# Kernel tuning notes

Hardware: AMD Instinct MI355X
Metric: run time of the kernel (lower is better)

Reference implementation:

```python
import jax, jax.numpy as jnp
import numpy as np

N = 50000      # nodes
E = 800000     # edges (avg degree 16)
EL = 200000    # link-prediction pairs
IN = 128       # in_channels
HID = 128      # hidden_conv_2


def setup_inputs() -> dict:
    key = jax.random.key(0)
    ks = jax.random.split(key, 12)
    x = jax.random.normal(ks[0], (N, IN), dtype=jnp.float32)
    edge_index = jax.random.randint(ks[1], (2, E), 0, N, dtype=jnp.int64)
    edge_label_index = jax.random.randint(ks[2], (2, EL), 0, N, dtype=jnp.int64)
    H = jnp.zeros((N, HID), dtype=jnp.float32)
    s_in = 1.0 / np.sqrt(IN)
    s_h = 1.0 / np.sqrt(HID)
    # Stacked ChebConv (K=2) weights for gates [z, r, h]:
    # Wx*: convs on the input x (IN -> HID); Wh*: convs on the state H (HID -> HID)
    Wx0 = jax.random.uniform(ks[3], (3, IN, HID), jnp.float32, -s_in, s_in)
    Wx1 = jax.random.uniform(ks[4], (3, IN, HID), jnp.float32, -s_in, s_in)
    bx = jax.random.uniform(ks[5], (3, HID), jnp.float32, -s_in, s_in)
    Wh0 = jax.random.uniform(ks[6], (3, HID, HID), jnp.float32, -s_h, s_h)
    Wh1 = jax.random.uniform(ks[7], (3, HID, HID), jnp.float32, -s_h, s_h)
    bh = jax.random.uniform(ks[8], (3, HID), jnp.float32, -s_h, s_h)
    post_w = jax.random.uniform(ks[9], (HID, 2), jnp.float32, -s_h, s_h)
    post_b = jax.random.uniform(ks[10], (2,), jnp.float32, -s_h, s_h)
    return {"x": x, "edge_index": edge_index, "edge_label_index": edge_label_index,
            "H": H, "Wx0": Wx0, "Wx1": Wx1, "bx": bx,
            "Wh0": Wh0, "Wh1": Wh1, "bh": bh,
            "post_w": post_w, "post_b": post_b}


def _gconv_gru(x, H, edge_index, Wx0, Wx1, bx, Wh0, Wh1, bh):
    src, dst = edge_index[0], edge_index[1]
    # Symmetric-normalized ChebConv edge weights with lambda_max=2:
    # L_hat = L - I = -D^{-1/2} A D^{-1/2}
    deg = jax.ops.segment_sum(jnp.ones(src.shape[0], x.dtype), src, num_segments=N)
    dinv = jnp.where(deg > 0, jax.lax.rsqrt(jnp.maximum(deg, 1e-12)), 0.0)
    norm = -(dinv[src] * dinv[dst])  # [E]

    def prop(v):  # L_hat @ v via gather-scale-scatter
        return jax.ops.segment_sum(v[src] * norm[:, None], dst, num_segments=N)

    px = prop(x)   # shared Tx_1 for all three x-convs
    pH = prop(H)

    def cheb_x(g):
        return x @ Wx0[g] + px @ Wx1[g] + bx[g]

    def cheb_h(v, pv, g):
        return v @ Wh0[g] + pv @ Wh1[g] + bh[g]

    Z = jax.nn.sigmoid(cheb_x(0) + cheb_h(H, pH, 0))
    R = jax.nn.sigmoid(cheb_x(1) + cheb_h(H, pH, 1))
    HR = H * R
    Ht = jnp.tanh(cheb_x(2) + cheb_h(HR, prop(HR), 2))
    return Z * H + (1.0 - Z) * Ht


def reference(x, edge_index, edge_label_index, H,
              Wx0, Wx1, bx, Wh0, Wh1, bh, post_w, post_b):
    h = _gconv_gru(x, H, edge_index, Wx0, Wx1, bx, Wh0, Wh1, bh)
    hidden = h  # detached copy in the original
    hr = jax.nn.relu(h)
    h_src = hr[edge_label_index[0]]  # [EL, HID]
    h_dst = hr[edge_label_index[1]]
    had = h_src * h_dst
    scores = jnp.sum(had @ post_w + post_b, axis=-1)  # [EL]
    return scores, hidden
```

## Files before the change

kernel.cpp:

```cpp
#include <hip/hip_runtime.h>

#define N_NODES 50000
#define N_EDGES 800000
#define N_EL    200000
#define CH      128
#define NTILES  3125

typedef __attribute__((ext_vector_type(8))) short bf16x8;
typedef __attribute__((ext_vector_type(4))) float f32x4;

__device__ __forceinline__ unsigned short f2bf(float f){
  unsigned int u = __float_as_uint(f);
  unsigned int r = (u + 0x7fff + ((u >> 16) & 1)) >> 16;
  return (unsigned short)r;
}
__device__ __forceinline__ float bflo(unsigned int v){ return __uint_as_float(v << 16); }
__device__ __forceinline__ float bfhi(unsigned int v){ return __uint_as_float(v & 0xffff0000u); }
__device__ __forceinline__ float bf2f(unsigned short u){ return __uint_as_float(((unsigned int)u) << 16); }

__global__ void hist_kernel(const int* __restrict__ ei, int* deg, int* cnt){
  int i = blockIdx.x*blockDim.x + threadIdx.x;
  if (i < N_EDGES){
    atomicAdd(&deg[ei[i]], 1);
    atomicAdd(&cnt[ei[N_EDGES + i]], 1);
  }
}

__global__ void dinv_kernel(const int* __restrict__ deg, float* __restrict__ dinv){
  int i = blockIdx.x*blockDim.x + threadIdx.x;
  if (i < N_NODES){
    int d = deg[i];
    dinv[i] = d > 0 ? rsqrtf((float)d) : 0.0f;
  }
}

#define SCAN_NB 196

__global__ void scan_bsum(const int* __restrict__ cnt, int* __restrict__ bsum){
  __shared__ int sh[256];
  int i = blockIdx.x*256 + threadIdx.x;
  sh[threadIdx.x] = (i < N_NODES) ? cnt[i] : 0;
  __syncthreads();
  for (int off = 128; off >= 1; off >>= 1){
    if ((int)threadIdx.x < off) sh[threadIdx.x] += sh[threadIdx.x + off];
    __syncthreads();
  }
  if (threadIdx.x == 0) bsum[blockIdx.x] = sh[0];
}

__global__ void scan_boff(const int* __restrict__ bsum, int* __restrict__ boff){
  __shared__ int sh[256];
  int t = threadIdx.x;
  int v = (t < SCAN_NB) ? bsum[t] : 0;
  sh[t] = v;
  __syncthreads();
  for (int off = 1; off < 256; off <<= 1){
    int tv = (t >= off) ? sh[t - off] : 0;
    __syncthreads();
    sh[t] += tv;
    __syncthreads();
  }
  if (t < SCAN_NB) boff[t] = sh[t] - v;
}

__global__ void scan_final(const int* __restrict__ cnt, const int* __restrict__ boff,
                           int* __restrict__ rowoff, int* __restrict__ cursor){
  __shared__ int sh[256];
  int t = threadIdx.x;
  int i = blockIdx.x*256 + t;
  int v = (i < N_NODES) ? cnt[i] : 0;
  sh[t] = v;
  __syncthreads();
  for (int off = 1; off < 256; off <<= 1){
    int tv = (t >= off) ? sh[t - off] : 0;
    __syncthreads();
    sh[t] += tv;
    __syncthreads();
  }
  int o = boff[blockIdx.x] + sh[t] - v;
  if (i < N_NODES){ rowoff[i] = o; cursor[i] = o; }
  if (i == N_NODES - 1) rowoff[N_NODES] = N_EDGES;
}

__global__ void scatter_kernel(const int* __restrict__ ei, const float* __restrict__ dinv,
                               int* cursor, int* __restrict__ csr_src,
                               float* __restrict__ csr_norm){
  int i = blockIdx.x*blockDim.x + threadIdx.x;
  if (i < N_EDGES){
    int s = ei[i];
    int d = ei[N_EDGES + i];
    int pos = atomicAdd(&cursor[d], 1);
    csr_src[pos]  = s;
    csr_norm[pos] = -(dinv[s] * dinv[d]);
  }
}

__global__ void cvt_xH(const float* __restrict__ x, const float* __restrict__ H,
                       unsigned short* __restrict__ xH){
  const int Q = (N_NODES*CH)/4;
  int i = blockIdx.x*blockDim.x + threadIdx.x;
  if (i >= 2*Q) return;
  const float* src = (i < Q) ? x : H;
  int off = (i < Q) ? i : i - Q;
  float4 v = ((const float4*)src)[off];
  int node = off >> 5, cg = off & 31;
  uint2 o;
  o.x = (unsigned int)f2bf(v.x) | ((unsigned int)f2bf(v.y) << 16);
  o.y = (unsigned int)f2bf(v.z) | ((unsigned int)f2bf(v.w) << 16);
  *(uint2*)(xH + (size_t)node*256 + ((i < Q) ? 0 : 128) + cg*4) = o;
}

__global__ void cvt_w(const float* __restrict__ Wx0, const float* __restrict__ Wx1,
                      const float* __restrict__ Wh0, const float* __restrict__ Wh1,
                      unsigned short* __restrict__ wt){
  int i = blockIdx.x*blockDim.x + threadIdx.x;
  if (i >= 12*128*128) return;
  int m = i >> 14;
  int r = i & 16383;
  int col = r >> 7, k = r & 127;
  const float* W[4] = {Wx0, Wx1, Wh0, Wh1};
  const float* src = W[m/3] + (m%3)*16384;
  wt[i] = f2bf(src[k*128 + col]);
}

__global__ void prop_x2(const int* __restrict__ rowoff, const int* __restrict__ csr_src,
                        const float* __restrict__ csr_norm,
                        const unsigned short* __restrict__ xH,
                        unsigned short* __restrict__ px, unsigned short* __restrict__ pH){
  int node = blockIdx.x*4 + ((int)threadIdx.x >> 6);
  if (node >= N_NODES) return;
  int lane = threadIdx.x & 63;
  int half = lane >> 5, il = lane & 31;
  const unsigned short* base = xH + half*128 + il*4;
  int beg = rowoff[node], end = rowoff[node+1];
  float a0 = 0.f, a1 = 0.f, a2 = 0.f, a3 = 0.f;
  int k = beg;
  for (; k + 4 <= end; k += 4){
    int s0 = csr_src[k], s1 = csr_src[k+1], s2 = csr_src[k+2], s3 = csr_src[k+3];
    float w0 = csr_norm[k], w1 = csr_norm[k+1], w2 = csr_norm[k+2], w3 = csr_norm[k+3];
    uint2 v0 = *(const uint2*)(base + (size_t)s0*256);
    uint2 v1 = *(const uint2*)(base + (size_t)s1*256);
    uint2 v2 = *(const uint2*)(base + (size_t)s2*256);
    uint2 v3 = *(const uint2*)(base + (size_t)s3*256);
    a0 += w0*bflo(v0.x) + w1*bflo(v1.x) + w2*bflo(v2.x) + w3*bflo(v3.x);
    a1 += w0*bfhi(v0.x) + w1*bfhi(v1.x) + w2*bfhi(v2.x) + w3*bfhi(v3.x);
    a2 += w0*bflo(v0.y) + w1*bflo(v1.y) + w2*bflo(v2.y) + w3*bflo(v3.y);
    a3 += w0*bfhi(v0.y) + w1*bfhi(v1.y) + w2*bfhi(v2.y) + w3*bfhi(v3.y);
  }
  for (; k < end; ++k){
    int s = csr_src[k];
    float w = csr_norm[k];
    uint2 v = *(const uint2*)(base + (size_t)s*256);
    a0 += w*bflo(v.x); a1 += w*bfhi(v.x);
    a2 += w*bflo(v.y); a3 += w*bfhi(v.y);
  }
  uint2 o;
  o.x = (unsigned int)f2bf(a0) | ((unsigned int)f2bf(a1) << 16);
  o.y = (unsigned int)f2bf(a2) | ((unsigned int)f2bf(a3) << 16);
  unsigned short* O = (half ? pH : px) + (size_t)node*CH + il*4;
  *(uint2*)O = o;
}

__global__ void prop_one(const int* __restrict__ rowoff, const int* __restrict__ csr_src,
                         const float* __restrict__ csr_norm,
                         const unsigned short* __restrict__ V,
                         unsigned short* __restrict__ O){
  int node = blockIdx.x*4 + ((int)threadIdx.x >> 6);
  if (node >= N_NODES) return;
  int lane = threadIdx.x & 63;
  const unsigned short* base = V + lane*2;
  int beg = rowoff[node], end = rowoff[node+1];
  float a0 = 0.f, a1 = 0.f;
  int k = beg;
  for (; k + 4 <= end; k += 4){
    int s0 = csr_src[k], s1 = csr_src[k+1], s2 = csr_src[k+2], s3 = csr_src[k+3];
    float w0 = csr_norm[k], w1 = csr_norm[k+1], w2 = csr_norm[k+2], w3 = csr_norm[k+3];
    unsigned int v0 = *(const unsigned int*)(base + (size_t)s0*256);
    unsigned int v1 = *(const unsigned int*)(base + (size_t)s1*256);
    unsigned int v2 = *(const unsigned int*)(base + (size_t)s2*256);
    unsigned int v3 = *(const unsigned int*)(base + (size_t)s3*256);
    a0 += w0*bflo(v0) + w1*bflo(v1) + w2*bflo(v2) + w3*bflo(v3);
    a1 += w0*bfhi(v0) + w1*bfhi(v1) + w2*bfhi(v2) + w3*bfhi(v3);
  }
  for (; k < end; ++k){
    int s = csr_src[k];
    float w = csr_norm[k];
    unsigned int v = *(const unsigned int*)(base + (size_t)s*256);
    a0 += w*bflo(v); a1 += w*bfhi(v);
  }
  *(unsigned int*)(O + (size_t)node*CH + lane*2) =
      (unsigned int)f2bf(a0) | ((unsigned int)f2bf(a1) << 16);
}

__launch_bounds__(512, 2)
__global__ void mfma_gates2(unsigned short* xH,
                            const unsigned short* __restrict__ px,
                            const unsigned short* __restrict__ pH,
                            const unsigned short* __restrict__ wt,
                            const float* __restrict__ bx, const float* __restrict__ bh,
                            unsigned short* __restrict__ zb,
                            float* __restrict__ pre2){
  const int M = 128*128;
  int lane = threadIdx.x & 63;
  int w    = threadIdx.x >> 6;
  int lr   = lane & 15;
  int kq   = lane >> 4;
  int mycol = w*16 + lr;

  const unsigned short* Am[4] = {xH, px, xH + 128, pH};
  const int strA[4] = {256, 128, 256, 128};

  bf16x8 BZ[16], BR[16], BP[8];
  #pragma unroll
  for (int t = 0; t < 4; ++t){
    #pragma unroll
    for (int q = 0; q < 4; ++q){
      const unsigned short* base = wt + (size_t)(t*3)*M + (size_t)mycol*CH + q*32 + kq*8;
      BZ[t*4+q] = *(const bf16x8*)(base);
      BR[t*4+q] = *(const bf16x8*)(base + M);
      if (t < 2) BP[t*4+q] = *(const bf16x8*)(base + 2*M);
    }
  }

  float bsZ = bx[mycol]       + bh[mycol];
  float bsR = bx[128 + mycol] + bh[128 + mycol];
  float bsP = bx[256 + mycol];

  for (int tile = blockIdx.x; tile < NTILES; tile += gridDim.x){
    int r0 = tile * 16;
    int rA = r0 + lr;
    f32x4 accZ = (f32x4){0.f,0.f,0.f,0.f};
    f32x4 accR = (f32x4){0.f,0.f,0.f,0.f};
    f32x4 accP = (f32x4){0.f,0.f,0.f,0.f};
    #pragma unroll
    for (int t = 0; t < 4; ++t){
      const unsigned short* Ap = Am[t] + (size_t)rA*strA[t] + kq*8;
      #pragma unroll
      for (int q = 0; q < 4; ++q){
        bf16x8 a = *(const bf16x8*)(Ap + q*32);
        accZ = __builtin_amdgcn_mfma_f32_16x16x32_bf16(a, BZ[t*4+q], accZ, 0, 0, 0);
        accR = __builtin_amdgcn_mfma_f32_16x16x32_bf16(a, BR[t*4+q], accR, 0, 0, 0);
        if (t < 2)
          accP = __builtin_amdgcn_mfma_f32_16x16x32_bf16(a, BP[t*4+q], accP, 0, 0, 0);
      }
    }
    #pragma unroll
    for (int j = 0; j < 4; ++j){
      int row = r0 + kq*4 + j;
      size_t ro = (size_t)row*CH + mycol;
      size_t rh = (size_t)row*256 + 128 + mycol;
      float z = 1.0f/(1.0f + __expf(-(accZ[j] + bsZ)));
      float r = 1.0f/(1.0f + __expf(-(accR[j] + bsR)));
      float h = bf2f(xH[rh]);
      zb[ro]   = f2bf(z);
      xH[rh]   = f2bf(h * r);
      pre2[ro] = accP[j] + bsP;
    }
  }
}

__launch_bounds__(512, 2)
__global__ void mfma_final2(const unsigned short* __restrict__ hr,
                            const unsigned short* __restrict__ phr,
                            const unsigned short* __restrict__ B0,
                            const unsigned short* __restrict__ B1,
                            const float* __restrict__ bias,
                            const float* __restrict__ Hp, const float* __restrict__ pre2,
                            const unsigned short* __restrict__ zb,
                            float* __restrict__ hidden,
                            unsigned short* __restrict__ relu_b){
  int lane = threadIdx.x & 63;
  int w    = threadIdx.x >> 6;
  int lr   = lane & 15;
  int kq   = lane >> 4;
  int mycol = w*16 + lr;

  const unsigned short* Am[2] = {hr, phr};
  const int strA[2] = {256, 128};

  bf16x8 BF[8];
  #pragma unroll
  for (int t = 0; t < 2; ++t){
    #pragma unroll
    for (int q = 0; q < 4; ++q){
      const unsigned short* B = t ? B1 : B0;
      BF[t*4+q] = *(const bf16x8*)(B + (size_t)mycol*CH + q*32 + kq*8);
    }
  }
  float bs = bias[mycol];

  for (int tile = blockIdx.x; tile < NTILES; tile += gridDim.x){
    int r0 = tile * 16;
    int rA = r0 + lr;
    f32x4 acc0 = (f32x4){0.f,0.f,0.f,0.f};
    f32x4 acc1 = (f32x4){0.f,0.f,0.f,0.f};
    #pragma unroll
    for (int q = 0; q < 4; ++q){
      bf16x8 a0 = *(const bf16x8*)(Am[0] + (size_t)rA*256 + q*32 + kq*8);
      bf16x8 a1 = *(const bf16x8*)(Am[1] + (size_t)rA*128 + q*32 + kq*8);
      acc0 = __builtin_amdgcn_mfma_f32_16x16x32_bf16(a0, BF[q],   acc0, 0, 0, 0);
      acc1 = __builtin_amdgcn_mfma_f32_16x16x32_bf16(a1, BF[4+q], acc1, 0, 0, 0);
    }
    #pragma unroll
    for (int j = 0; j < 4; ++j){
      int row = r0 + kq*4 + j;
      size_t o = (size_t)row*CH + mycol;
      float ht = tanhf(acc0[j] + acc1[j] + bs + pre2[o]);
      float z  = bf2f(zb[o]);
      float h  = z*Hp[o] + (1.0f - z)*ht;
      hidden[o] = h;
      relu_b[o] = f2bf(fmaxf(h, 0.0f));
    }
  }
}

__global__ void scores_bf16(const int* __restrict__ eli, const unsigned short* __restrict__ hr,
                            const float* __restrict__ pw, const float* __restrict__ pb,
                            float* __restrict__ out){
  __shared__ float sw[CH];
  int t = threadIdx.x;
  if (t < CH) sw[t] = pw[2*t] + pw[2*t + 1];
  __syncthreads();
  int pair = blockIdx.x*16 + (t >> 4);
  if (pair >= N_EL) return;
  int il = t & 15;
  int a = eli[pair];
  int b = eli[N_EL + pair];
  bf16x8 va = *(const bf16x8*)(hr + (size_t)a*CH + il*8);
  bf16x8 vb = *(const bf16x8*)(hr + (size_t)b*CH + il*8);
  float s = 0.f;
  #pragma unroll
  for (int j = 0; j < 8; ++j){
    s += bf2f((unsigned short)va[j]) * bf2f((unsigned short)vb[j]) * sw[il*8 + j];
  }
  s += __shfl_xor(s, 1, 64);
  s += __shfl_xor(s, 2, 64);
  s += __shfl_xor(s, 4, 64);
  s += __shfl_xor(s, 8, 64);
  if (il == 0) out[pair] = s + pb[0] + pb[1];
}

extern "C" void kernel_launch(void* const* d_in, const int* in_sizes, int n_in,
                              void* d_out, int out_size, void* d_ws, size_t ws_size,
                              hipStream_t stream) {
  const float* x   = (const float*)d_in[0];
  const int*   ei  = (const int*)d_in[1];
  const int*   eli = (const int*)d_in[2];
  const float* H   = (const float*)d_in[3];
  const float* Wx0 = (const float*)d_in[4];
  const float* Wx1 = (const float*)d_in[5];
  const float* bx  = (const float*)d_in[6];
  const float* Wh0 = (const float*)d_in[7];
  const float* Wh1 = (const float*)d_in[8];
  const float* bh  = (const float*)d_in[9];
  const float* pw  = (const float*)d_in[10];
  const float* pb  = (const float*)d_in[11];
  float* out    = (float*)d_out;
  float* scores = out;
  float* hidden = out + N_EL;

  char* w = (char*)d_ws;
  auto alloc = [&](size_t b){ void* p = (void*)w; w += (b + 255) & ~(size_t)255; return p; };
  int*   deg      = (int*)  alloc((size_t)N_NODES*4);
  int*   cnt      = (int*)  alloc((size_t)N_NODES*4);
  float* dinv     = (float*)alloc((size_t)N_NODES*4);
  int*   rowoff   = (int*)  alloc((size_t)(N_NODES+1)*4);
  int*   cursor   = (int*)  alloc((size_t)N_NODES*4);
  int*   bsum     = (int*)  alloc((size_t)SCAN_NB*4);
  int*   boff     = (int*)  alloc((size_t)SCAN_NB*4);
  int*   csr_src  = (int*)  alloc((size_t)N_EDGES*4);
  float* csr_norm = (float*)alloc((size_t)N_EDGES*4);
  unsigned short* wt  = (unsigned short*)alloc((size_t)12*128*128*2);
  unsigned short* xHb = (unsigned short*)alloc((size_t)N_NODES*256*2);
  unsigned short* pxb = (unsigned short*)alloc((size_t)N_NODES*CH*2);
  unsigned short* pHb = (unsigned short*)alloc((size_t)N_NODES*CH*2);
  unsigned short* zbb = (unsigned short*)alloc((size_t)N_NODES*CH*2);
  float* pre2 = (float*)alloc((size_t)N_NODES*CH*4);
  unsigned short* pHRb   = pHb;
  unsigned short* relu_b = pxb;

  hipMemsetAsync(deg, 0, (size_t)N_NODES*4, stream);
  hipMemsetAsync(cnt, 0, (size_t)N_NODES*4, stream);

  hist_kernel<<<(N_EDGES+255)/256, 256, 0, stream>>>(ei, deg, cnt);
  dinv_kernel<<<(N_NODES+255)/256, 256, 0, stream>>>(deg, dinv);
  scan_bsum <<<SCAN_NB, 256, 0, stream>>>(cnt, bsum);
  scan_boff <<<1, 256, 0, stream>>>(bsum, boff);
  scan_final<<<SCAN_NB, 256, 0, stream>>>(cnt, boff, rowoff, cursor);
  scatter_kernel<<<(N_EDGES+255)/256, 256, 0, stream>>>(ei, dinv, cursor, csr_src, csr_norm);

  cvt_xH<<<(((N_NODES*CH)/4)*2 + 255)/256, 256, 0, stream>>>(x, H, xHb);
  cvt_w <<<(12*128*128 + 255)/256, 256, 0, stream>>>(Wx0, Wx1, Wh0, Wh1, wt);

  prop_x2<<<(N_NODES+3)/4, 256, 0, stream>>>(rowoff, csr_src, csr_norm, xHb, pxb, pHb);

  const size_t M = 128*128;
  mfma_gates2<<<512, 512, 0, stream>>>(xHb, pxb, pHb, wt, bx, bh, zbb, pre2);
  prop_one<<<(N_NODES+3)/4, 256, 0, stream>>>(rowoff, csr_src, csr_norm, xHb + 128, pHRb);
  mfma_final2<<<512, 512, 0, stream>>>(xHb + 128, pHRb, wt + 8*M, wt + 11*M,
      bh + 256, H, pre2, zbb, hidden, relu_b);

  scores_bf16<<<(N_EL+15)/16, 256, 0, stream>>>(eli, relu_b, pw, pb, scores);
}
```

Before: 467.0 us.

## Split gate GEMMs across grid by gate and column half, widen gather unroll

Splits the fused Z/R/P gate MFMA kernel into a 2D grid where each block handles one gate flavor and one half of the output columns, with 32-row tiles and zero-padded weights. H*R is written to a separate dense buffer instead of back into the interleaved xH array, so prop_one and the final GEMM read a contiguous 128-wide layout. Both propagation kernels unroll the edge gather to 8 to raise memory-level parallelism. The split adds redundant A-tile reads across flavors and column halves, and MFMA work on zero padding for the candidate gate, in exchange for more parallelism and lower register pressure.

```diff
diff --git a/kernel.cpp b/kernel.cpp
--- a/kernel.cpp
+++ b/kernel.cpp
@@ -4,7 +4,7 @@
 #define N_EDGES 800000
 #define N_EL    200000
 #define CH      128
-#define NTILES  3125
+#define NT32    1563
 
 typedef __attribute__((ext_vector_type(8))) short bf16x8;
 typedef __attribute__((ext_vector_type(4))) float f32x4;
@@ -112,15 +112,25 @@
 
 __global__ void cvt_w(const float* __restrict__ Wx0, const float* __restrict__ Wx1,
                       const float* __restrict__ Wh0, const float* __restrict__ Wh1,
-                      unsigned short* __restrict__ wt){
+                      unsigned short* __restrict__ wtg){
   int i = blockIdx.x*blockDim.x + threadIdx.x;
-  if (i >= 12*128*128) return;
+  if (i >= 14*16384) return;
   int m = i >> 14;
   int r = i & 16383;
   int col = r >> 7, k = r & 127;
-  const float* W[4] = {Wx0, Wx1, Wh0, Wh1};
-  const float* src = W[m/3] + (m%3)*16384;
-  wt[i] = f2bf(src[k*128 + col]);
+  float v;
+  if (m < 12){
+    int g = m >> 2, t = m & 3;
+    int so = g*16384 + k*128 + col;
+    if (t == 0)      v = Wx0[so];
+    else if (t == 1) v = Wx1[so];
+    else if (t == 2) v = (g < 2) ? Wh0[so] : 0.f;
+    else             v = (g < 2) ? Wh1[so] : 0.f;
+  } else {
+    int so = 2*16384 + k*128 + col;
+    v = (m == 12) ? Wh0[so] : Wh1[so];
+  }
+  wtg[(size_t)m*16384 + col*128 + k] = f2bf(v);
 }
 
 __global__ void prop_x2(const int* __restrict__ rowoff, const int* __restrict__ csr_src,
@@ -135,17 +145,17 @@
   int beg = rowoff[node], end = rowoff[node+1];
   float a0 = 0.f, a1 = 0.f, a2 = 0.f, a3 = 0.f;
   int k = beg;
-  for (; k + 4 <= end; k += 4){
-    int s0 = csr_src[k], s1 = csr_src[k+1], s2 = csr_src[k+2], s3 = csr_src[k+3];
-    float w0 = csr_norm[k], w1 = csr_norm[k+1], w2 = csr_norm[k+2], w3 = csr_norm[k+3];
-    uint2 v0 = *(const uint2*)(base + (size_t)s0*256);
-    uint2 v1 = *(const uint2*)(base + (size_t)s1*256);
-    uint2 v2 = *(const uint2*)(base + (size_t)s2*256);
-    uint2 v3 = *(const uint2*)(base + (size_t)s3*256);
-    a0 += w0*bflo(v0.x) + w1*bflo(v1.x) + w2*bflo(v2.x) + w3*bflo(v3.x);
-    a1 += w0*bfhi(v0.x) + w1*bfhi(v1.x) + w2*bfhi(v2.x) + w3*bfhi(v3.x);
-    a2 += w0*bflo(v0.y) + w1*bflo(v1.y) + w2*bflo(v2.y) + w3*bflo(v3.y);
-    a3 += w0*bfhi(v0.y) + w1*bfhi(v1.y) + w2*bfhi(v2.y) + w3*bfhi(v3.y);
+  for (; k + 8 <= end; k += 8){
+    int s[8]; float wn[8]; uint2 v[8];
+    #pragma unroll
+    for (int u = 0; u < 8; ++u){ s[u] = csr_src[k+u]; wn[u] = csr_norm[k+u]; }
+    #pragma unroll
+    for (int u = 0; u < 8; ++u) v[u] = *(const uint2*)(base + (size_t)s[u]*256);
+    #pragma unroll
+    for (int u = 0; u < 8; ++u){
+      a0 += wn[u]*bflo(v[u].x); a1 += wn[u]*bfhi(v[u].x);
+      a2 += wn[u]*bflo(v[u].y); a3 += wn[u]*bfhi(v[u].y);
+    }
   }
   for (; k < end; ++k){
     int s = csr_src[k];
@@ -172,144 +182,158 @@
   int beg = rowoff[node], end = rowoff[node+1];
   float a0 = 0.f, a1 = 0.f;
   int k = beg;
-  for (; k + 4 <= end; k += 4){
-    int s0 = csr_src[k], s1 = csr_src[k+1], s2 = csr_src[k+2], s3 = csr_src[k+3];
-    float w0 = csr_norm[k], w1 = csr_norm[k+1], w2 = csr_norm[k+2], w3 = csr_norm[k+3];
-    unsigned int v0 = *(const unsigned int*)(base + (size_t)s0*256);
-    unsigned int v1 = *(const unsigned int*)(base + (size_t)s1*256);
-    unsigned int v2 = *(const unsigned int*)(base + (size_t)s2*256);
-    unsigned int v3 = *(const unsigned int*)(base + (size_t)s3*256);
-    a0 += w0*bflo(v0) + w1*bflo(v1) + w2*bflo(v2) + w3*bflo(v3);
-    a1 += w0*bfhi(v0) + w1*bfhi(v1) + w2*bfhi(v2) + w3*bfhi(v3);
+  for (; k + 8 <= end; k += 8){
+    int s[8]; float wn[8]; unsigned int v[8];
+    #pragma unroll
+    for (int u = 0; u < 8; ++u){ s[u] = csr_src[k+u]; wn[u] = csr_norm[k+u]; }
+    #pragma unroll
+    for (int u = 0; u < 8; ++u) v[u] = *(const unsigned int*)(base + (size_t)s[u]*CH);
+    #pragma unroll
+    for (int u = 0; u < 8; ++u){
+      a0 += wn[u]*bflo(v[u]); a1 += wn[u]*bfhi(v[u]);
+    }
   }
   for (; k < end; ++k){
     int s = csr_src[k];
     float w = csr_norm[k];
-    unsigned int v = *(const unsigned int*)(base + (size_t)s*256);
+    unsigned int v = *(const unsigned int*)(base + (size_t)s*CH);
     a0 += w*bflo(v); a1 += w*bfhi(v);
   }
   *(unsigned int*)(O + (size_t)node*CH + lane*2) =
       (unsigned int)f2bf(a0) | ((unsigned int)f2bf(a1) << 16);
 }
 
-__launch_bounds__(512, 2)
-__global__ void mfma_gates2(unsigned short* xH,
+__launch_bounds__(256, 4)
+__global__ void mfma_gsplit(const unsigned short* __restrict__ xH,
                             const unsigned short* __restrict__ px,
                             const unsigned short* __restrict__ pH,
-                            const unsigned short* __restrict__ wt,
+                            const unsigned short* __restrict__ wtg,
                             const float* __restrict__ bx, const float* __restrict__ bh,
                             unsigned short* __restrict__ zb,
+                            unsigned short* __restrict__ hrb,
                             float* __restrict__ pre2){
-  const int M = 128*128;
+  const int flavor  = blockIdx.y >> 1;
+  const int colhalf = blockIdx.y & 1;
   int lane = threadIdx.x & 63;
   int w    = threadIdx.x >> 6;
   int lr   = lane & 15;
   int kq   = lane >> 4;
-  int mycol = w*16 + lr;
+  int mycol = colhalf*64 + w*16 + lr;
 
   const unsigned short* Am[4] = {xH, px, xH + 128, pH};
   const int strA[4] = {256, 128, 256, 128};
 
-  bf16x8 BZ[16], BR[16], BP[8];
+  bf16x8 BF[16];
   #pragma unroll
-  for (int t = 0; t < 4; ++t){
-    #pragma unroll
-    for (int q = 0; q < 4; ++q){
-      const unsigned short* base = wt + (size_t)(t*3)*M + (size_t)mycol*CH + q*32 + kq*8;
-      BZ[t*4+q] = *(const bf16x8*)(base);
-      BR[t*4+q] = *(const bf16x8*)(base + M);
-      if (t < 2) BP[t*4+q] = *(const bf16x8*)(base + 2*M);
-    }
-  }
-
-  float bsZ = bx[mycol]       + bh[mycol];
-  float bsR = bx[128 + mycol] + bh[128 + mycol];
-  float bsP = bx[256 + mycol];
-
-  for (int tile = blockIdx.x; tile < NTILES; tile += gridDim.x){
-    int r0 = tile * 16;
-    int rA = r0 + lr;
-    f32x4 accZ = (f32x4){0.f,0.f,0.f,0.f};
-    f32x4 accR = (f32x4){0.f,0.f,0.f,0.f};
-    f32x4 accP = (f32x4){0.f,0.f,0.f,0.f};
+  for (int t = 0; t < 4; ++t)
+    #pragma unroll
+    for (int q = 0; q < 4; ++q)
+      BF[t*4+q] = *(const bf16x8*)(wtg + (size_t)(flavor*4 + t)*16384
+                                   + (size_t)mycol*CH + q*32 + kq*8);
+
+  float bs = (flavor == 0) ? bx[mycol] + bh[mycol]
+           : (flavor == 1) ? bx[128 + mycol] + bh[128 + mycol]
+                           : bx[256 + mycol];
+
+  for (int tile = blockIdx.x; tile < NT32; tile += gridDim.x){
+    int r0 = tile * 32;
+    int rA0 = min(r0 + lr,      N_NODES - 1);
+    int rA1 = min(r0 + 16 + lr, N_NODES - 1);
+    f32x4 acc0 = (f32x4){0.f,0.f,0.f,0.f};
+    f32x4 acc1 = (f32x4){0.f,0.f,0.f,0.f};
     #pragma unroll
     for (int t = 0; t < 4; ++t){
-      const unsigned short* Ap = Am[t] + (size_t)rA*strA[t] + kq*8;
+      const unsigned short* Ap = Am[t];
+      const int st = strA[t];
       #pragma unroll
       for (int q = 0; q < 4; ++q){
-        bf16x8 a = *(const bf16x8*)(Ap + q*32);
-        accZ = __builtin_amdgcn_mfma_f32_16x16x32_bf16(a, BZ[t*4+q], accZ, 0, 0, 0);
-        accR = __builtin_amdgcn_mfma_f32_16x16x32_bf16(a, BR[t*4+q], accR, 0, 0, 0);
-        if (t < 2)
-          accP = __builtin_amdgcn_mfma_f32_16x16x32_bf16(a, BP[t*4+q], accP, 0, 0, 0);
+        bf16x8 a0 = *(const bf16x8*)(Ap + (size_t)rA0*st + q*32 + kq*8);
+        bf16x8 a1 = *(const bf16x8*)(Ap + (size_t)rA1*st + q*32 + kq*8);
+        acc0 = __builtin_amdgcn_mfma_f32_16x16x32_bf16(a0, BF[t*4+q], acc0, 0, 0, 0);
+        acc1 = __builtin_amdgcn_mfma_f32_16x16x32_bf16(a1, BF[t*4+q], acc1, 0, 0, 0);
       }
     }
     #pragma unroll
-    for (int j = 0; j < 4; ++j){
-      int row = r0 + kq*4 + j;
-      size_t ro = (size_t)row*CH + mycol;
-      size_t rh = (size_t)row*256 + 128 + mycol;
-      float z = 1.0f/(1.0f + __expf(-(accZ[j] + bsZ)));
-      float r = 1.0f/(1.0f + __expf(-(accR[j] + bsR)));
-      float h = bf2f(xH[rh]);
-      zb[ro]   = f2bf(z);
-      xH[rh]   = f2bf(h * r);
-      pre2[ro] = accP[j] + bsP;
-    }
-  }
-}
-
-__launch_bounds__(512, 2)
-__global__ void mfma_final2(const unsigned short* __restrict__ hr,
+    for (int rg = 0; rg < 2; ++rg){
+      const f32x4& ac = rg ? acc1 : acc0;
+      #pragma unroll
+      for (int j = 0; j < 4; ++j){
+        int row = r0 + rg*16 + kq*4 + j;
+        if (row >= N_NODES) continue;
+        size_t o = (size_t)row*CH + mycol;
+        float v = ac[j] + bs;
+        if (flavor == 0){
+          zb[o] = f2bf(1.0f/(1.0f + __expf(-v)));
+        } else if (flavor == 1){
+          float h = bf2f(xH[(size_t)row*256 + 128 + mycol]);
+          hrb[o] = f2bf(h * (1.0f/(1.0f + __expf(-v))));
+        } else {
+          pre2[o] = v;
+        }
+      }
+    }
+  }
+}
+
+__launch_bounds__(256, 4)
+__global__ void mfma_fsplit(const unsigned short* __restrict__ hr,
                             const unsigned short* __restrict__ phr,
-                            const unsigned short* __restrict__ B0,
-                            const unsigned short* __restrict__ B1,
-                            const float* __restrict__ bias,
+                            const unsigned short* __restrict__ wtg,
+                            const float* __restrict__ bh,
                             const float* __restrict__ Hp, const float* __restrict__ pre2,
                             const unsigned short* __restrict__ zb,
                             float* __restrict__ hidden,
                             unsigned short* __restrict__ relu_b){
+  const int colhalf = blockIdx.y;
   int lane = threadIdx.x & 63;
   int w    = threadIdx.x >> 6;
   int lr   = lane & 15;
   int kq   = lane >> 4;
-  int mycol = w*16 + lr;
+  int mycol = colhalf*64 + w*16 + lr;
 
   const unsigned short* Am[2] = {hr, phr};
-  const int strA[2] = {256, 128};
 
   bf16x8 BF[8];
   #pragma unroll
-  for (int t = 0; t < 2; ++t){
-    #pragma unroll
-    for (int q = 0; q < 4; ++q){
-      const unsigned short* B = t ? B1 : B0;
-      BF[t*4+q] = *(const bf16x8*)(B + (size_t)mycol*CH + q*32 + kq*8);
-    }
-  }
-  float bs = bias[mycol];
-
-  for (int tile = blockIdx.x; tile < NTILES; tile += gridDim.x){
-    int r0 = tile * 16;
-    int rA = r0 + lr;
+  for (int t = 0; t < 2; ++t)
+    #pragma unroll
+    for (int q = 0; q < 4; ++q)
+      BF[t*4+q] = *(const bf16x8*)(wtg + (size_t)(12 + t)*16384
+                                   + (size_t)mycol*CH + q*32 + kq*8);
+
+  float bs = bh[256 + mycol];
+
+  for (int tile = blockIdx.x; tile < NT32; tile += gridDim.x){
+    int r0 = tile * 32;
+    int rA0 = min(r0 + lr,      N_NODES - 1);
+    int rA1 = min(r0 + 16 + lr, N_NODES - 1);
     f32x4 acc0 = (f32x4){0.f,0.f,0.f,0.f};
     f32x4 acc1 = (f32x4){0.f,0.f,0.f,0.f};
     #pragma unroll
-    for (int q = 0; q < 4; ++q){
-      bf16x8 a0 = *(const bf16x8*)(Am[0] + (size_t)rA*256 + q*32 + kq*8);
-      bf16x8 a1 = *(const bf16x8*)(Am[1] + (size_t)rA*128 + q*32 + kq*8);
-      acc0 = __builtin_amdgcn_mfma_f32_16x16x32_bf16(a0, BF[q],   acc0, 0, 0, 0);
-      acc1 = __builtin_amdgcn_mfma_f32_16x16x32_bf16(a1, BF[4+q], acc1, 0, 0, 0);
-    }
-    #pragma unroll
-    for (int j = 0; j < 4; ++j){
-      int row = r0 + kq*4 + j;
-      size_t o = (size_t)row*CH + mycol;
-      float ht = tanhf(acc0[j] + acc1[j] + bs + pre2[o]);
-      float z  = bf2f(zb[o]);
-      float h  = z*Hp[o] + (1.0f - z)*ht;
-      hidden[o] = h;
-      relu_b[o] = f2bf(fmaxf(h, 0.0f));
+    for (int t = 0; t < 2; ++t){
+      const unsigned short* Ap = Am[t];
+      #pragma unroll
+      for (int q = 0; q < 4; ++q){
+        bf16x8 a0 = *(const bf16x8*)(Ap + (size_t)rA0*CH + q*32 + kq*8);
+        bf16x8 a1 = *(const bf16x8*)(Ap + (size_t)rA1*CH + q*32 + kq*8);
+        acc0 = __builtin_amdgcn_mfma_f32_16x16x32_bf16(a0, BF[t*4+q], acc0, 0, 0, 0);
+        acc1 = __builtin_amdgcn_mfma_f32_16x16x32_bf16(a1, BF[t*4+q], acc1, 0, 0, 0);
+      }
+    }
+    #pragma unroll
+    for (int rg = 0; rg < 2; ++rg){
+      const f32x4& ac = rg ? acc1 : acc0;
+      #pragma unroll
+      for (int j = 0; j < 4; ++j){
+        int row = r0 + rg*16 + kq*4 + j;
+        if (row >= N_NODES) continue;
+        size_t o = (size_t)row*CH + mycol;
+        float ht = tanhf(ac[j] + bs + pre2[o]);
+        float z  = bf2f(zb[o]);
+        float h  = z*Hp[o] + (1.0f - z)*ht;
+        hidden[o] = h;
+        relu_b[o] = f2bf(fmaxf(h, 0.0f));
+      }
     }
   }
 }
@@ -370,11 +394,12 @@
   int*   boff     = (int*)  alloc((size_t)SCAN_NB*4);
   int*   csr_src  = (int*)  alloc((size_t)N_EDGES*4);
   float* csr_norm = (float*)alloc((size_t)N_EDGES*4);
-  unsigned short* wt  = (unsigned short*)alloc((size_t)12*128*128*2);
+  unsigned short* wtg = (unsigned short*)alloc((size_t)14*16384*2);
   unsigned short* xHb = (unsigned short*)alloc((size_t)N_NODES*256*2);
   unsigned short* pxb = (unsigned short*)alloc((size_t)N_NODES*CH*2);
   unsigned short* pHb = (unsigned short*)alloc((size_t)N_NODES*CH*2);
   unsigned short* zbb = (unsigned short*)alloc((size_t)N_NODES*CH*2);
+  unsigned short* hrb = (unsigned short*)alloc((size_t)N_NODES*CH*2);
   float* pre2 = (float*)alloc((size_t)N_NODES*CH*4);
   unsigned short* pHRb   = pHb;
   unsigned short* relu_b = pxb;
@@ -390,15 +415,15 @@
   scatter_kernel<<<(N_EDGES+255)/256, 256, 0, stream>>>(ei, dinv, cursor, csr_src, csr_norm);
 
   cvt_xH<<<(((N_NODES*CH)/4)*2 + 255)/256, 256, 0, stream>>>(x, H, xHb);
-  cvt_w <<<(12*128*128 + 255)/256, 256, 0, stream>>>(Wx0, Wx1, Wh0, Wh1, wt);
+  cvt_w <<<(14*16384 + 255)/256, 256, 0, stream>>>(Wx0, Wx1, Wh0, Wh1, wtg);
 
   prop_x2<<<(N_NODES+3)/4, 256, 0, stream>>>(rowoff, csr_src, csr_norm, xHb, pxb, pHb);
 
-  const size_t M = 128*128;
-  mfma_gates2<<<512, 512, 0, stream>>>(xHb, pxb, pHb, wt, bx, bh, zbb, pre2);
-  prop_one<<<(N_NODES+3)/4, 256, 0, stream>>>(rowoff, csr_src, csr_norm, xHb + 128, pHRb);
-  mfma_final2<<<512, 512, 0, stream>>>(xHb + 128, pHRb, wt + 8*M, wt + 11*M,
-      bh + 256, H, pre2, zbb, hidden, relu_b);
+  mfma_gsplit<<<dim3(96, 6), 256, 0, stream>>>(xHb, pxb, pHb, wtg, bx, bh,
+                                               zbb, hrb, pre2);
+  prop_one<<<(N_NODES+3)/4, 256, 0, stream>>>(rowoff, csr_src, csr_norm, hrb, pHRb);
+  mfma_fsplit<<<dim3(192, 2), 256, 0, stream>>>(hrb, pHRb, wtg, bh,
+                                                H, pre2, zbb, hidden, relu_b);
 
   scores_bf16<<<(N_EL+15)/16, 256, 0, stream>>>(eli, relu_b, pw, pb, scores);
 }
```

Result: slower. 620.6 us (+32.9%).
